# Kernel tuning notes

Measured on AMD Instinct MI355X. Metric: run time of the kernel, lower is better.

The kernel has to match this reference:

```python
import jax, jax.numpy as jnp
import numpy as np
from jax import lax

B, CIN, COUT, H, W = 4, 256, 256, 64, 64
K = 3  # kernel size
PAD = 1
STRIDE = 1


def setup_inputs() -> dict:
    key = jax.random.key(0)
    k1, k2, k3, k4 = jax.random.split(key, 4)
    x = jax.random.normal(k1, (B, CIN, H, W), dtype=jnp.float32)
    # small offset weights so learned offsets are modest (original init is zeros)
    offset_w = jax.random.normal(k2, (3 * K * K, CIN, K, K), dtype=jnp.float32) * 0.01
    offset_b = jax.random.normal(k3, (3 * K * K,), dtype=jnp.float32) * 0.01
    dcn_w = jax.random.normal(k4, (COUT, CIN, K, K), dtype=jnp.float32) * (1.0 / np.sqrt(CIN * K * K))
    return {"x": x, "offset_w": offset_w, "offset_b": offset_b, "dcn_w": dcn_w}


def _dcnv2(x, offset_w, offset_b, dcn_w):
    b, c, h, w = x.shape
    kk = K * K
    # offset conv (standard 3x3, stride 1, pad 1)
    o = lax.conv_general_dilated(
        x, offset_w, (STRIDE, STRIDE), ((PAD, PAD), (PAD, PAD)),
        dimension_numbers=("NCHW", "OIHW", "NCHW"))
    o = o + offset_b[None, :, None, None]
    ho, wo = o.shape[2], o.shape[3]
    off = o[:, : 2 * kk].reshape(b, kk, 2, ho, wo)  # pairs are (dy, dx)
    dy, dx = off[:, :, 0], off[:, :, 1]             # [b,kk,ho,wo]
    mask = jax.nn.sigmoid(o[:, 2 * kk:])            # [b,kk,ho,wo]

    ki, kj = jnp.meshgrid(jnp.arange(K), jnp.arange(K), indexing="ij")
    ki = ki.reshape(kk).astype(jnp.float32)
    kj = kj.reshape(kk).astype(jnp.float32)
    base_y = (jnp.arange(ho, dtype=jnp.float32) * STRIDE - PAD)[None, None, :, None] + ki[None, :, None, None]
    base_x = (jnp.arange(wo, dtype=jnp.float32) * STRIDE - PAD)[None, None, None, :] + kj[None, :, None, None]
    py = base_y + dy  # [b,kk,ho,wo] sampling y
    px = base_x + dx  # sampling x

    y0 = jnp.floor(py)
    x0 = jnp.floor(px)
    wy = py - y0  # bilinear fractional weights
    wx = px - x0
    y0i = y0.astype(jnp.int32)
    x0i = x0.astype(jnp.int32)

    xT = x.transpose(0, 2, 3, 1)  # [b,h,w,c] for channel-last gathers
    bidx = jnp.arange(b)[:, None, None, None]

    def gather(yi, xi):
        # zero padding outside the image
        valid = (yi >= 0) & (yi < h) & (xi >= 0) & (xi < w)
        yc = jnp.clip(yi, 0, h - 1)
        xc = jnp.clip(xi, 0, w - 1)
        v = xT[bidx, yc, xc]  # [b,kk,ho,wo,c]
        return v * valid[..., None].astype(x.dtype)

    g00 = gather(y0i, x0i)
    g01 = gather(y0i, x0i + 1)
    g10 = gather(y0i + 1, x0i)
    g11 = gather(y0i + 1, x0i + 1)

    wy_ = wy[..., None]
    wx_ = wx[..., None]
    sampled = (g00 * (1 - wy_) * (1 - wx_) + g01 * (1 - wy_) * wx_
               + g10 * wy_ * (1 - wx_) + g11 * wy_ * wx_)
    sampled = sampled * mask[..., None]  # modulation

    wk = dcn_w.reshape(dcn_w.shape[0], c, kk)  # [o,c,kk]
    return jnp.einsum("bkhwc,ock->bohw", sampled, wk)


def reference(x, offset_w, offset_b, dcn_w):
    return _dcnv2(x, offset_w, offset_b, dcn_w)
```

## Files before the change

kernel.cpp:

```cpp
#include <hip/hip_runtime.h>
#include <hip/hip_bf16.h>
#include <stdint.h>
#include <math.h>

#define KDIM 2304

typedef __attribute__((ext_vector_type(8))) short bf16x8;
typedef __attribute__((ext_vector_type(4))) float f32x4;

__device__ inline unsigned short f2bf(float f) {
  union { float f; unsigned int u; } v; v.f = f;
  unsigned int u = v.u;
  unsigned int r = (u + 0x7FFFu + ((u >> 16) & 1u)) >> 16;
  return (unsigned short)r;
}
__device__ inline float bf2f(unsigned short h) {
  union { unsigned int u; float f; } v; v.u = ((unsigned int)h) << 16;
  return v.f;
}

__device__ inline void gl2lds16(const void* g, void* l) {
  __builtin_amdgcn_global_load_lds((const __attribute__((address_space(1))) void*)g,
                                   (__attribute__((address_space(3))) void*)l,
                                   16, 0, 0);
}

#define GLOAD16(dst, ptr) \
  asm volatile("global_load_dwordx4 %0, %1, off" : "=v"(dst) : "v"(ptr))

__global__ __launch_bounds__(256) void k_prep(const float* __restrict__ x,
                                              unsigned short* __restrict__ xTb,
                                              const float* __restrict__ dcn_w,
                                              const float* __restrict__ offset_w,
                                              unsigned short* __restrict__ Wpk,
                                              unsigned short* __restrict__ Wob,
                                              unsigned short* __restrict__ zp) {
  __shared__ float tile[32][65];
  int bx = (int)blockIdx.x;
  int t = threadIdx.x;
  if (bx < 2048) {
    int pt = bx & 127, ct = (bx >> 7) & 3, b = bx >> 9;
    int p0 = pt * 32, c0 = ct * 64;
    const float* xb = x + ((size_t)b << 20);
#pragma unroll
    for (int i = 0; i < 2; ++i) {
      int idx = t + i * 256;
      int c = idx >> 3, pq = idx & 7;
      float4 v = *(const float4*)(xb + ((size_t)(c0 + c) << 12) + p0 + pq * 4);
      tile[pq * 4 + 0][c] = v.x;
      tile[pq * 4 + 1][c] = v.y;
      tile[pq * 4 + 2][c] = v.z;
      tile[pq * 4 + 3][c] = v.w;
    }
    __syncthreads();
    unsigned short* ob = xTb + ((size_t)b << 20);
#pragma unroll
    for (int i = 0; i < 2; ++i) {
      int idx = t + i * 256;
      int p = idx >> 4, cg = idx & 15;
      ushort4 o;
      o.x = f2bf(tile[p][cg * 4 + 0]);
      o.y = f2bf(tile[p][cg * 4 + 1]);
      o.z = f2bf(tile[p][cg * 4 + 2]);
      o.w = f2bf(tile[p][cg * 4 + 3]);
      *(ushort4*)(ob + (((size_t)(p0 + p)) << 8) + c0 + cg * 4) = o;
    }
  } else {
    int gid = (bx - 2048) * 256 + t;
    const int N1 = 72 * 8192;
    const int N2 = 32 * KDIM;
    if (gid < N1) {
      int j = gid & 7;
      int lane = (gid >> 3) & 63;
      int mb = (gid >> 9) & 15;
      int kc = gid >> 13;
      int row = mb * 16 + (lane & 15);
      int gk = kc * 32 + ((lane >> 4) << 3) + j;
      int c = gk & 255, kidx = gk >> 8;
      Wpk[gid] = f2bf(dcn_w[((size_t)(row * 256 + c)) * 9 + kidx]);
    } else if (gid < N1 + N2) {
      int g = gid - N1;
      int ch = g / KDIM, k = g % KDIM;
      int kidx = k >> 8, c = k & 255;
      Wob[g] = (ch < 27) ? f2bf(offset_w[((size_t)(ch * 256 + c)) * 9 + kidx])
                         : (unsigned short)0;
    } else if (gid < N1 + N2 + 128) {
      zp[gid - N1 - N2] = 0;
    }
  }
}

__global__ __launch_bounds__(256) void k_offs(const unsigned short* __restrict__ xTb,
                                              const unsigned short* __restrict__ Wob,
                                              const unsigned short* __restrict__ zp,
                                              const float* __restrict__ offb,
                                              float* __restrict__ SW) {
  __shared__ unsigned short As[4][32 * 32];
  __shared__ unsigned short Bs[4][32 * 32];
  __shared__ float Os[32][33];
  int t = threadIdx.x;
  int wv = t >> 6, lane = t & 63;
  int bid = (int)blockIdx.x;
  int swz = (bid & 7) * 64 + (bid >> 3);
  int n0 = swz * 32;

  int r0 = (t >> 2) & 31, coff = (t & 3) * 8;
  int rowA = n0 + r0;
  int b_ = rowA >> 12, hw = rowA & 4095, h = hw >> 6, w = hw & 63;
  int rB = ((t - 128) >> 2) & 31;

  f32x4 acc = {};

  auto stage = [&](int kt) {
    int buf = kt & 3;
    int k0 = kt * 32;
    int kidx = k0 >> 8, c0 = k0 & 255;
    if (t < 128) {
      int di = kidx / 3 - 1, dj = kidx % 3 - 1;
      int y = h + di, xx = w + dj;
      const unsigned short* g = (y >= 0 && y < 64 && xx >= 0 && xx < 64)
          ? xTb + (((((size_t)b_) << 12) + (y << 6) + xx) << 8) + c0 + coff
          : zp;
      gl2lds16(g, (char*)As[buf] + wv * 1024);
    } else {
      const unsigned short* gB = Wob + (size_t)rB * KDIM + k0 + coff;
      gl2lds16(gB, (char*)Bs[buf] + (wv - 2) * 1024);
    }
  };

  stage(0); stage(1); stage(2);

  int mf = wv & 1, nf = wv >> 1;
  for (int kt = 0; kt < 72; ++kt) {
    if (kt <= 69)      asm volatile("s_waitcnt vmcnt(2)" ::: "memory");
    else if (kt == 70) asm volatile("s_waitcnt vmcnt(1)" ::: "memory");
    else               asm volatile("s_waitcnt vmcnt(0)" ::: "memory");
    asm volatile("s_barrier" ::: "memory");
    if (kt + 3 < 72) stage(kt + 3);
    int buf = kt & 3;
    bf16x8 aF = *(const bf16x8*)(As[buf] + (mf * 16 + (lane & 15)) * 32 + (lane >> 4) * 8);
    bf16x8 bF = *(const bf16x8*)(Bs[buf] + (nf * 16 + (lane & 15)) * 32 + (lane >> 4) * 8);
    acc = __builtin_amdgcn_mfma_f32_16x16x32_bf16(aF, bF, acc, 0, 0, 0);
  }

  int quad = lane >> 4, cl = lane & 15;
#pragma unroll
  for (int r = 0; r < 4; ++r)
    Os[mf * 16 + quad * 4 + r][nf * 16 + cl] = acc[r];
  __syncthreads();

  for (int item = t; item < 288; item += 256) {
    int bl = item & 31, k = item >> 5;
    int bhw = n0 + bl;
    int h_ = (bhw >> 6) & 63, w_ = bhw & 63;
    float dy = Os[bl][2 * k]     + offb[2 * k];
    float dx = Os[bl][2 * k + 1] + offb[2 * k + 1];
    float mv = Os[bl][18 + k]    + offb[18 + k];
    float mask = 1.0f / (1.0f + expf(-mv));

    float py = (float)(h_ - 1 + k / 3) + dy;
    float px = (float)(w_ - 1 + k % 3) + dx;
    float y0f = floorf(py), x0f = floorf(px);
    float wy = py - y0f, wx = px - x0f;
    int y0 = (int)y0f, x0 = (int)x0f;
    int y1 = y0 + 1, x1 = x0 + 1;

    float vy0 = (y0 >= 0 && y0 < 64) ? 1.f : 0.f;
    float vy1 = (y1 >= 0 && y1 < 64) ? 1.f : 0.f;
    float vx0 = (x0 >= 0 && x0 < 64) ? 1.f : 0.f;
    float vx1 = (x1 >= 0 && x1 < 64) ? 1.f : 0.f;
    int y0c = min(max(y0, 0), 63), y1c = min(max(y1, 0), 63);
    int x0c = min(max(x0, 0), 63), x1c = min(max(x1, 0), 63);

    float4 wv4;
    wv4.x = (1.f - wy) * (1.f - wx) * vy0 * vx0 * mask;
    wv4.y = (1.f - wy) * wx * vy0 * vx1 * mask;
    wv4.z = wy * (1.f - wx) * vy1 * vx0 * mask;
    wv4.w = wy * wx * vy1 * vx1 * mask;
    uint4 ov;
    ov.x = (unsigned)(((y0c << 6) + x0c) << 8);
    ov.y = (unsigned)(((y0c << 6) + x1c) << 8);
    ov.z = (unsigned)(((y1c << 6) + x0c) << 8);
    ov.w = (unsigned)(((y1c << 6) + x1c) << 8);

    float* p = SW + (size_t)(k * 16384 + bhw) * 8;
    *(float4*)p = wv4;
    *(uint4*)(p + 4) = ov;
  }
}

#define PHASE(PH, Q, AF, BUF, WB, WM)                                          \
  do {                                                                         \
    if (((PH) & 3) == 0) {                                                     \
      int g_ = (PH) >> 2;                                                      \
      wv4 = *(const float4*)(SWL + (size_t)(g_ * 128 + r * 2) * 4);            \
      ov  = *(const uint4*)(SWL + (size_t)(g_ * 128 + r * 2 + 1) * 4);         \
    } else if (((PH) & 3) == 2 && (PH) < 32) {                                 \
      ov  = *(const uint4*)(SWL + (size_t)((((PH) >> 2) + 1) * 128 + r * 2 + 1) * 4); \
    }                                                                          \
    asm volatile("s_waitcnt vmcnt(" #WB ")" ::: "memory");                     \
    __builtin_amdgcn_sched_barrier(0);                                         \
    float s_[8];                                                               \
    _Pragma("unroll")                                                          \
    for (int j_ = 0; j_ < 8; ++j_)                                             \
      s_[j_] = wv4.x * bf2f((unsigned short)Q[0][j_]) +                        \
               wv4.y * bf2f((unsigned short)Q[1][j_]) +                        \
               wv4.z * bf2f((unsigned short)Q[2][j_]) +                        \
               wv4.w * bf2f((unsigned short)Q[3][j_]);                         \
    union { __hip_bfloat162 h2[4]; bf16x8 v; } pk_;                            \
    pk_.h2[0] = __float22bfloat162_rn(make_float2(s_[0], s_[1]));              \
    pk_.h2[1] = __float22bfloat162_rn(make_float2(s_[2], s_[3]));              \
    pk_.h2[2] = __float22bfloat162_rn(make_float2(s_[4], s_[5]));              \
    pk_.h2[3] = __float22bfloat162_rn(make_float2(s_[6], s_[7]));              \
    *(bf16x8*)(&Bs[BUF][s_th][bsw]) = pk_.v;                                   \
    if ((PH) < 34) {                                                           \
      int kn0_ = 2 * (PH) + 4;                                                 \
      unsigned c_ = (unsigned)((((kn0_ & 7) + s_th) << 5) + gg * 8);           \
      GLOAD16(Q[0], xb + ov.x + c_);                                           \
      GLOAD16(Q[1], xb + ov.y + c_);                                           \
      GLOAD16(Q[2], xb + ov.z + c_);                                           \
      GLOAD16(Q[3], xb + ov.w + c_);                                           \
    }                                                                          \
    asm volatile("s_waitcnt vmcnt(" #WM ") lgkmcnt(0)\n\ts_barrier" ::: "memory"); \
    __builtin_amdgcn_sched_barrier(0);                                         \
    _Pragma("unroll")                                                          \
    for (int s2_ = 0; s2_ < 2; ++s2_) {                                        \
      bf16x8 bF0_ = *(const bf16x8*)(                                          \
          &Bs[BUF][s2_][(wn * 32 + (lane & 15)) * 56 + (lane >> 4) * 8]);      \
      bf16x8 bF1_ = *(const bf16x8*)(                                          \
          &Bs[BUF][s2_][(wn * 32 + 16 + (lane & 15)) * 56 + (lane >> 4) * 8]); \
      _Pragma("unroll")                                                        \
      for (int i_ = 0; i_ < 4; ++i_) {                                         \
        acc[i_][0] = __builtin_amdgcn_mfma_f32_16x16x32_bf16(                  \
            AF[s2_ * 4 + i_], bF0_, acc[i_][0], 0, 0, 0);                      \
        acc[i_][1] = __builtin_amdgcn_mfma_f32_16x16x32_bf16(                  \
            AF[s2_ * 4 + i_], bF1_, acc[i_][1], 0, 0, 0);                      \
      }                                                                        \
    }                                                                          \
    if ((PH) < 34) {                                                           \
      _Pragma("unroll")                                                        \
      for (int i_ = 0; i_ < 8; ++i_) {                                         \
        const unsigned short* ap_ =                                            \
            wpBase + ((size_t)((2 * (PH) + 4 + (i_ >> 2)) * 16 + (i_ & 3))) * 512; \
        GLOAD16(AF[i_], ap_);                                                  \
      }                                                                        \
    }                                                                          \
  } while (0)

__global__ __launch_bounds__(512, 2) void k_fused(const unsigned short* __restrict__ Wpk,
                                                  const unsigned short* __restrict__ xTb,
                                                  const float* __restrict__ SW,
                                                  float* __restrict__ out) {
  __shared__ __align__(16) unsigned short Bs[2][2][64 * 56];
  __shared__ __align__(16) float SWL[1152 * 4];
  int t = threadIdx.x;
  int wv = t >> 6, lane = t & 63;
  int wm = wv & 3, wn = wv >> 2;
  int bid = (int)blockIdx.x;
  int swz = (bid & 7) * 32 + (bid >> 3);
  int n0 = swz * 64;
  int b  = n0 >> 12;
  const unsigned short* xb = xTb + ((size_t)b << 20);

  int r = t >> 3;
  int u = t & 7;
  int s_th = u & 1, gg = u >> 1;
  int bsw = r * 56 + gg * 8;

  const unsigned short* wpBase = Wpk + ((size_t)(wm * 4 * 64 + lane)) * 8;

  f32x4 acc[4][2] = {};

  {
#pragma unroll
    for (int i = 0; i < 3; ++i) {
      int hs = t + i * 512;
      if (hs < 1152) {
        int grp = hs >> 7, row = (hs >> 1) & 63, hh = hs & 1;
        const float* src = SW + ((size_t)(grp * 16384 + n0 + row)) * 8 + hh * 4;
        char* dstbase = (char*)SWL + ((size_t)((t & ~63) + i * 512)) * 16;
        gl2lds16(src, dstbase);
      }
    }
  }
  asm volatile("s_waitcnt vmcnt(0)" ::: "memory");
  __builtin_amdgcn_s_barrier();

  float4 wv4; uint4 ov;
  wv4 = *(const float4*)(SWL + (size_t)(r * 2) * 4);
  ov  = *(const uint4*)(SWL + (size_t)(r * 2 + 1) * 4);

  bf16x8 qA[4], qB[4];
  bf16x8 aFA[8], aFB[8];

  {
    unsigned cA = (unsigned)((s_th << 5) + gg * 8);
    GLOAD16(qA[0], xb + ov.x + cA);
    GLOAD16(qA[1], xb + ov.y + cA);
    GLOAD16(qA[2], xb + ov.z + cA);
    GLOAD16(qA[3], xb + ov.w + cA);
#pragma unroll
    for (int i = 0; i < 8; ++i) {
      const unsigned short* ap = wpBase + ((size_t)(((i >> 2)) * 16 + (i & 3))) * 512;
      GLOAD16(aFA[i], ap);
    }
    unsigned cB = (unsigned)(((2 + s_th) << 5) + gg * 8);
    GLOAD16(qB[0], xb + ov.x + cB);
    GLOAD16(qB[1], xb + ov.y + cB);
    GLOAD16(qB[2], xb + ov.z + cB);
    GLOAD16(qB[3], xb + ov.w + cB);
#pragma unroll
    for (int i = 0; i < 8; ++i) {
      const unsigned short* ap = wpBase + ((size_t)((2 + (i >> 2)) * 16 + (i & 3))) * 512;
      GLOAD16(aFB[i], ap);
    }
  }

  for (int ph = 0; ph < 34; ph += 2) {
    PHASE(ph,     qA, aFA, 0, 20, 16);
    PHASE(ph + 1, qB, aFB, 1, 20, 16);
  }
  PHASE(34, qA, aFA, 0, 20, 12);
  PHASE(35, qB, aFB, 1, 8, 0);

  int quad = lane >> 4, cl = lane & 15;
  float* ob = out + (((size_t)b) << 20);
#pragma unroll
  for (int i = 0; i < 4; ++i) {
    int mbase = wm * 64 + i * 16 + quad * 4;
#pragma unroll
    for (int j = 0; j < 2; ++j) {
      int hw = (n0 & 4095) + wn * 32 + j * 16 + cl;
      float* op = ob + hw;
#pragma unroll
      for (int rr = 0; rr < 4; ++rr)
        op[((size_t)(mbase + rr)) << 12] = acc[i][j][rr];
    }
  }
}

extern "C" void kernel_launch(void* const* d_in, const int* in_sizes, int n_in,
                              void* d_out, int out_size, void* d_ws, size_t ws_size,
                              hipStream_t stream) {
  const float* x        = (const float*)d_in[0];
  const float* offset_w = (const float*)d_in[1];
  const float* offset_b = (const float*)d_in[2];
  const float* dcn_w    = (const float*)d_in[3];
  float* out = (float*)d_out;

  char* ws = (char*)d_ws;
  size_t off = 0;
  auto carve = [&](size_t bytes) -> void* {
    void* p = ws + off;
    off += (bytes + 255) & ~(size_t)255;
    return p;
  };
  unsigned short* xTb = (unsigned short*)carve(4ull * 64 * 64 * 256 * 2);
  unsigned short* Wpk = (unsigned short*)carve(72ull * 8192 * 2);
  unsigned short* Wob = (unsigned short*)carve(32ull * KDIM * 2);
  unsigned short* zp  = (unsigned short*)carve(256);
  float*          SW  = (float*)carve(9ull * 16384 * 8 * 4);
  (void)ws_size; (void)in_sizes; (void)n_in; (void)out_size;

  const int WPREP_BLOCKS = (72 * 8192 + 32 * KDIM + 128 + 255) / 256;
  k_prep<<<dim3(2048 + WPREP_BLOCKS), 256, 0, stream>>>(
      x, xTb, dcn_w, offset_w, Wpk, Wob, zp);
  k_offs<<<dim3(512), 256, 0, stream>>>(xTb, Wob, zp, offset_b, SW);
  k_fused<<<dim3(256), 512, 0, stream>>>(Wpk, xTb, SW, out);
}
```

Before: 131.6 us.

## Widen K-step to 128 in fused DCN GEMM and double offset-conv tile

The fused deformable-sampling GEMM now processes 128 channels per phase instead of 64, in 18 phases with one barrier each. Each thread samples 16 channels per phase, and weight-fragment loads are interleaved per 32-channel chunk with finer vmcnt waits. The offset-conv kernel moves to 64-row tiles with 512 threads, 64-wide K steps and an XOR-swizzled LDS layout, halving the block count and barrier count. This cuts synchronization overhead and improves reuse, at the cost of more registers (16 weight fragments, 8 gather registers) and larger LDS use, which may reduce occupancy.

```diff
diff --git a/kernel.cpp b/kernel.cpp
--- a/kernel.cpp
+++ b/kernel.cpp
@@ -27,6 +27,12 @@
 
 #define GLOAD16(dst, ptr) \
   asm volatile("global_load_dwordx4 %0, %1, off" : "=v"(dst) : "v"(ptr))
+
+#define WAITV(N)                                              \
+  do {                                                        \
+    asm volatile("s_waitcnt vmcnt(" #N ")" ::: "memory");     \
+    __builtin_amdgcn_sched_barrier(0);                        \
+  } while (0)
 
 __global__ __launch_bounds__(256) void k_prep(const float* __restrict__ x,
                                               unsigned short* __restrict__ xTb,
@@ -90,57 +96,75 @@
   }
 }
 
-__global__ __launch_bounds__(256) void k_offs(const unsigned short* __restrict__ xTb,
+__global__ __launch_bounds__(512) void k_offs(const unsigned short* __restrict__ xTb,
                                               const unsigned short* __restrict__ Wob,
                                               const unsigned short* __restrict__ zp,
                                               const float* __restrict__ offb,
                                               float* __restrict__ SW) {
-  __shared__ unsigned short As[4][32 * 32];
-  __shared__ unsigned short Bs[4][32 * 32];
-  __shared__ float Os[32][33];
+  __shared__ unsigned short As[4][64 * 64];
+  __shared__ unsigned short Bsf[4][32 * 64];
+  __shared__ float Os[64][33];
   int t = threadIdx.x;
   int wv = t >> 6, lane = t & 63;
   int bid = (int)blockIdx.x;
-  int swz = (bid & 7) * 64 + (bid >> 3);
-  int n0 = swz * 32;
-
-  int r0 = (t >> 2) & 31, coff = (t & 3) * 8;
-  int rowA = n0 + r0;
+  int swz = (bid & 7) * 32 + (bid >> 3);
+  int n0 = swz * 64;
+
+  int ra = t >> 3, ua = t & 7;
+  int kpA = ((ua ^ (ra & 7)) << 3);
+  int rowA = n0 + ra;
   int b_ = rowA >> 12, hw = rowA & 4095, h = hw >> 6, w = hw & 63;
-  int rB = ((t - 128) >> 2) & 31;
+  int rb = (t >> 3) & 31;
+  int kpB = (((t & 7) ^ (rb & 7)) << 3);
 
   f32x4 acc = {};
 
   auto stage = [&](int kt) {
     int buf = kt & 3;
-    int k0 = kt * 32;
+    int k0 = kt * 64;
     int kidx = k0 >> 8, c0 = k0 & 255;
-    if (t < 128) {
+    {
       int di = kidx / 3 - 1, dj = kidx % 3 - 1;
       int y = h + di, xx = w + dj;
       const unsigned short* g = (y >= 0 && y < 64 && xx >= 0 && xx < 64)
-          ? xTb + (((((size_t)b_) << 12) + (y << 6) + xx) << 8) + c0 + coff
+          ? xTb + (((((size_t)b_) << 12) + (y << 6) + xx) << 8) + c0 + kpA
           : zp;
       gl2lds16(g, (char*)As[buf] + wv * 1024);
+    }
+    if (t < 256) {
+      const unsigned short* gB = Wob + (size_t)rb * KDIM + k0 + kpB;
+      gl2lds16(gB, (char*)Bsf[buf] + wv * 1024);
+    }
+  };
+
+  stage(0); stage(1); stage(2);
+
+  int mf = wv & 3, nf = wv >> 2;
+  int arow = mf * 16 + (lane & 15);
+  int brow = nf * 16 + (lane & 15);
+  int q4 = lane >> 4;
+  for (int kt = 0; kt < 36; ++kt) {
+    if (kt <= 33) {
+      if (wv < 4) asm volatile("s_waitcnt vmcnt(4)" ::: "memory");
+      else        asm volatile("s_waitcnt vmcnt(2)" ::: "memory");
+    } else if (kt == 34) {
+      if (wv < 4) asm volatile("s_waitcnt vmcnt(2)" ::: "memory");
+      else        asm volatile("s_waitcnt vmcnt(1)" ::: "memory");
     } else {
-      const unsigned short* gB = Wob + (size_t)rB * KDIM + k0 + coff;
-      gl2lds16(gB, (char*)Bs[buf] + (wv - 2) * 1024);
-    }
-  };
-
-  stage(0); stage(1); stage(2);
-
-  int mf = wv & 1, nf = wv >> 1;
-  for (int kt = 0; kt < 72; ++kt) {
-    if (kt <= 69)      asm volatile("s_waitcnt vmcnt(2)" ::: "memory");
-    else if (kt == 70) asm volatile("s_waitcnt vmcnt(1)" ::: "memory");
-    else               asm volatile("s_waitcnt vmcnt(0)" ::: "memory");
+      asm volatile("s_waitcnt vmcnt(0)" ::: "memory");
+    }
     asm volatile("s_barrier" ::: "memory");
-    if (kt + 3 < 72) stage(kt + 3);
+    if (kt + 3 < 36) stage(kt + 3);
     int buf = kt & 3;
-    bf16x8 aF = *(const bf16x8*)(As[buf] + (mf * 16 + (lane & 15)) * 32 + (lane >> 4) * 8);
-    bf16x8 bF = *(const bf16x8*)(Bs[buf] + (nf * 16 + (lane & 15)) * 32 + (lane >> 4) * 8);
-    acc = __builtin_amdgcn_mfma_f32_16x16x32_bf16(aF, bF, acc, 0, 0, 0);
+#pragma unroll
+    for (int cc = 0; cc < 2; ++cc) {
+      int kq = (cc << 2) + q4;
+      bf16x8 aF = *(const bf16x8*)((const char*)As[buf] +
+                                   arow * 128 + (((kq ^ (arow & 7))) << 4));
+      bf16x8 bF = *(const bf16x8*)((const char*)Bsf[buf] +
+                                   brow * 128 + (((kq ^ (brow & 7))) << 4));
+      acc = __builtin_amdgcn_mfma_f32_16x16x32_bf16(aF, bF, acc, 0, 0, 0);
+    }
   }
 
   int quad = lane >> 4, cl = lane & 15;
@@ -149,8 +173,8 @@
     Os[mf * 16 + quad * 4 + r][nf * 16 + cl] = acc[r];
   __syncthreads();
 
-  for (int item = t; item < 288; item += 256) {
-    int bl = item & 31, k = item >> 5;
+  for (int item = t; item < 576; item += 512) {
+    int bl = item & 63, k = item >> 6;
     int bhw = n0 + bl;
     int h_ = (bhw >> 6) & 63, w_ = bhw & 63;
     float dy = Os[bl][2 * k]     + offb[2 * k];
@@ -189,69 +213,85 @@
   }
 }
 
-#define PHASE(PH, Q, AF, BUF, WB, WM)                                          \
+#define FCHUNK(P, CC, BUF, ISSUE, W)                                           \
   do {                                                                         \
-    if (((PH) & 3) == 0) {                                                     \
-      int g_ = (PH) >> 2;                                                      \
-      wv4 = *(const float4*)(SWL + (size_t)(g_ * 128 + r * 2) * 4);            \
-      ov  = *(const uint4*)(SWL + (size_t)(g_ * 128 + r * 2 + 1) * 4);         \
-    } else if (((PH) & 3) == 2 && (PH) < 32) {                                 \
-      ov  = *(const uint4*)(SWL + (size_t)((((PH) >> 2) + 1) * 128 + r * 2 + 1) * 4); \
+    WAITV(W);                                                                  \
+    bf16x8 bF0_ = *(const bf16x8*)(                                            \
+        &Bs[BUF][(wn * 32 + (lane & 15)) * 136 + (CC) * 32 + (lane >> 4) * 8]);\
+    bf16x8 bF1_ = *(const bf16x8*)(                                            \
+        &Bs[BUF][(wn * 32 + 16 + (lane & 15)) * 136 + (CC) * 32 +              \
+                 (lane >> 4) * 8]);                                            \
+    _Pragma("unroll")                                                          \
+    for (int i_ = 0; i_ < 4; ++i_) {                                           \
+      acc[i_][0] = __builtin_amdgcn_mfma_f32_16x16x32_bf16(                    \
+          aF[(CC) * 4 + i_], bF0_, acc[i_][0], 0, 0, 0);                       \
+      acc[i_][1] = __builtin_amdgcn_mfma_f32_16x16x32_bf16(                    \
+          aF[(CC) * 4 + i_], bF1_, acc[i_][1], 0, 0, 0);                       \
     }                                                                          \
-    asm volatile("s_waitcnt vmcnt(" #WB ")" ::: "memory");                     \
+    if (ISSUE) {                                                               \
+      _Pragma("unroll")                                                        \
+      for (int i_ = 0; i_ < 4; ++i_)                                           \
+        GLOAD16(aF[(CC) * 4 + i_],                                             \
+                wpBase + ((size_t)((((P) + 1) * 4 + (CC)) * 16 + i_)) * 512);  \
+    }                                                                          \
+  } while (0)
+
+#define FPHASE(P, BUF, ISSUE, W0, W1, W2, W3)                                  \
+  do {                                                                         \
+    if ((((P) & 1) == 0) && (P) < 16) {                                        \
+      int g_ = ((P) >> 1) + 1;                                                 \
+      wv4n = *(const float4*)(SWL + (size_t)(g_ * 128 + r * 2) * 4);           \
+      ovn  = *(const uint4*)(SWL + (size_t)(g_ * 128 + r * 2 + 1) * 4);        \
+    }                                                                          \
+    WAITV(16);                                                                 \
+    float s_[16];                                                              \
+    _Pragma("unroll")                                                          \
+    for (int j_ = 0; j_ < 8; ++j_) {                                           \
+      s_[j_] = wv4.x * bf2f((unsigned short)q[0][j_]) +                        \
+               wv4.y * bf2f((unsigned short)q[1][j_]) +                        \
+               wv4.z * bf2f((unsigned short)q[2][j_]) +                        \
+               wv4.w * bf2f((unsigned short)q[3][j_]);                         \
+      s_[8 + j_] = wv4.x * bf2f((unsigned short)q[4][j_]) +                    \
+                   wv4.y * bf2f((unsigned short)q[5][j_]) +                    \
+                   wv4.z * bf2f((unsigned short)q[6][j_]) +                    \
+                   wv4.w * bf2f((unsigned short)q[7][j_]);                     \
+    }                                                                          \
+    union { __hip_bfloat162 h2[4]; bf16x8 v; } pka_, pkb_;                     \
+    pka_.h2[0] = __float22bfloat162_rn(make_float2(s_[0], s_[1]));             \
+    pka_.h2[1] = __float22bfloat162_rn(make_float2(s_[2], s_[3]));             \
+    pka_.h2[2] = __float22bfloat162_rn(make_float2(s_[4], s_[5]));             \
+    pka_.h2[3] = __float22bfloat162_rn(make_float2(s_[6], s_[7]));             \
+    pkb_.h2[0] = __float22bfloat162_rn(make_float2(s_[8], s_[9]));             \
+    pkb_.h2[1] = __float22bfloat162_rn(make_float2(s_[10], s_[11]));           \
+    pkb_.h2[2] = __float22bfloat162_rn(make_float2(s_[12], s_[13]));           \
+    pkb_.h2[3] = __float22bfloat162_rn(make_float2(s_[14], s_[15]));           \
+    *(bf16x8*)(&Bs[BUF][bsw])     = pka_.v;                                    \
+    *(bf16x8*)(&Bs[BUF][bsw + 8]) = pkb_.v;                                    \
+    if (ISSUE) {                                                               \
+      uint4 o_ = (((P) & 1) ? ovn : ov);                                       \
+      unsigned cb_ = (unsigned)((((((P) + 1)) & 1) << 7) + u * 16);            \
+      GLOAD16(q[0], xb + o_.x + cb_);                                          \
+      GLOAD16(q[1], xb + o_.y + cb_);                                          \
+      GLOAD16(q[2], xb + o_.z + cb_);                                          \
+      GLOAD16(q[3], xb + o_.w + cb_);                                          \
+      GLOAD16(q[4], xb + o_.x + cb_ + 8);                                      \
+      GLOAD16(q[5], xb + o_.y + cb_ + 8);                                      \
+      GLOAD16(q[6], xb + o_.z + cb_ + 8);                                      \
+      GLOAD16(q[7], xb + o_.w + cb_ + 8);                                      \
+    }                                                                          \
+    asm volatile("s_waitcnt lgkmcnt(0)\n\ts_barrier" ::: "memory");            \
     __builtin_amdgcn_sched_barrier(0);                                         \
-    float s_[8];                                                               \
-    _Pragma("unroll")                                                          \
-    for (int j_ = 0; j_ < 8; ++j_)                                             \
-      s_[j_] = wv4.x * bf2f((unsigned short)Q[0][j_]) +                        \
-               wv4.y * bf2f((unsigned short)Q[1][j_]) +                        \
-               wv4.z * bf2f((unsigned short)Q[2][j_]) +                        \
-               wv4.w * bf2f((unsigned short)Q[3][j_]);                         \
-    union { __hip_bfloat162 h2[4]; bf16x8 v; } pk_;                            \
-    pk_.h2[0] = __float22bfloat162_rn(make_float2(s_[0], s_[1]));              \
-    pk_.h2[1] = __float22bfloat162_rn(make_float2(s_[2], s_[3]));              \
-    pk_.h2[2] = __float22bfloat162_rn(make_float2(s_[4], s_[5]));              \
-    pk_.h2[3] = __float22bfloat162_rn(make_float2(s_[6], s_[7]));              \
-    *(bf16x8*)(&Bs[BUF][s_th][bsw]) = pk_.v;                                   \
-    if ((PH) < 34) {                                                           \
-      int kn0_ = 2 * (PH) + 4;                                                 \
-      unsigned c_ = (unsigned)((((kn0_ & 7) + s_th) << 5) + gg * 8);           \
-      GLOAD16(Q[0], xb + ov.x + c_);                                           \
-      GLOAD16(Q[1], xb + ov.y + c_);                                           \
-      GLOAD16(Q[2], xb + ov.z + c_);                                           \
-      GLOAD16(Q[3], xb + ov.w + c_);                                           \
-    }                                                                          \
-    asm volatile("s_waitcnt vmcnt(" #WM ") lgkmcnt(0)\n\ts_barrier" ::: "memory"); \
-    __builtin_amdgcn_sched_barrier(0);                                         \
-    _Pragma("unroll")                                                          \
-    for (int s2_ = 0; s2_ < 2; ++s2_) {                                        \
-      bf16x8 bF0_ = *(const bf16x8*)(                                          \
-          &Bs[BUF][s2_][(wn * 32 + (lane & 15)) * 56 + (lane >> 4) * 8]);      \
-      bf16x8 bF1_ = *(const bf16x8*)(                                          \
-          &Bs[BUF][s2_][(wn * 32 + 16 + (lane & 15)) * 56 + (lane >> 4) * 8]); \
-      _Pragma("unroll")                                                        \
-      for (int i_ = 0; i_ < 4; ++i_) {                                         \
-        acc[i_][0] = __builtin_amdgcn_mfma_f32_16x16x32_bf16(                  \
-            AF[s2_ * 4 + i_], bF0_, acc[i_][0], 0, 0, 0);                      \
-        acc[i_][1] = __builtin_amdgcn_mfma_f32_16x16x32_bf16(                  \
-            AF[s2_ * 4 + i_], bF1_, acc[i_][1], 0, 0, 0);                      \
-      }                                                                        \
-    }                                                                          \
-    if ((PH) < 34) {                                                           \
-      _Pragma("unroll")                                                        \
-      for (int i_ = 0; i_ < 8; ++i_) {                                         \
-        const unsigned short* ap_ =                                            \
-            wpBase + ((size_t)((2 * (PH) + 4 + (i_ >> 2)) * 16 + (i_ & 3))) * 512; \
-        GLOAD16(AF[i_], ap_);                                                  \
-      }                                                                        \
-    }                                                                          \
+    FCHUNK(P, 0, BUF, ISSUE, W0);                                              \
+    FCHUNK(P, 1, BUF, ISSUE, W1);                                              \
+    FCHUNK(P, 2, BUF, ISSUE, W2);                                              \
+    FCHUNK(P, 3, BUF, ISSUE, W3);                                              \
   } while (0)
 
 __global__ __launch_bounds__(512, 2) void k_fused(const unsigned short* __restrict__ Wpk,
                                                   const unsigned short* __restrict__ xTb,
                                                   const float* __restrict__ SW,
                                                   float* __restrict__ out) {
-  __shared__ __align__(16) unsigned short Bs[2][2][64 * 56];
+  __shared__ __align__(16) unsigned short Bs[2][64 * 136];
   __shared__ __align__(16) float SWL[1152 * 4];
   int t = threadIdx.x;
   int wv = t >> 6, lane = t & 63;
@@ -264,8 +304,7 @@
 
   int r = t >> 3;
   int u = t & 7;
-  int s_th = u & 1, gg = u >> 1;
-  int bsw = r * 56 + gg * 8;
+  int bsw = r * 136 + u * 16;
 
   const unsigned short* wpBase = Wpk + ((size_t)(wm * 4 * 64 + lane)) * 8;
 
@@ -286,42 +325,38 @@
   asm volatile("s_waitcnt vmcnt(0)" ::: "memory");
   __builtin_amdgcn_s_barrier();
 
-  float4 wv4; uint4 ov;
+  float4 wv4, wv4n; uint4 ov, ovn;
   wv4 = *(const float4*)(SWL + (size_t)(r * 2) * 4);
   ov  = *(const uint4*)(SWL + (size_t)(r * 2 + 1) * 4);
-
-  bf16x8 qA[4], qB[4];
-  bf16x8 aFA[8], aFB[8];
+  wv4n = wv4; ovn = ov;
+
+  bf16x8 q[8];
+  bf16x8 aF[16];
 
   {
-    unsigned cA = (unsigned)((s_th << 5) + gg * 8);
-    GLOAD16(qA[0], xb + ov.x + cA);
-    GLOAD16(qA[1], xb + ov.y + cA);
-    GLOAD16(qA[2], xb + ov.z + cA);
-    GLOAD16(qA[3], xb + ov.w + cA);
-#pragma unroll
-    for (int i = 0; i < 8; ++i) {
-      const unsigned short* ap = wpBase + ((size_t)(((i >> 2)) * 16 + (i & 3))) * 512;
-      GLOAD16(aFA[i], ap);
-    }
-    unsigned cB = (unsigned)(((2 + s_th) << 5) + gg * 8);
-    GLOAD16(qB[0], xb + ov.x + cB);
-    GLOAD16(qB[1], xb + ov.y + cB);
-    GLOAD16(qB[2], xb + ov.z + cB);
-    GLOAD16(qB[3], xb + ov.w + cB);
-#pragma unroll
-    for (int i = 0; i < 8; ++i) {
-      const unsigned short* ap = wpBase + ((size_t)((2 + (i >> 2)) * 16 + (i & 3))) * 512;
-      GLOAD16(aFB[i], ap);
-    }
-  }
-
-  for (int ph = 0; ph < 34; ph += 2) {
-    PHASE(ph,     qA, aFA, 0, 20, 16);
-    PHASE(ph + 1, qB, aFB, 1, 20, 16);
-  }
-  PHASE(34, qA, aFA, 0, 20, 12);
-  PHASE(35, qB, aFB, 1, 8, 0);
+    unsigned cb = (unsigned)(u * 16);
+    GLOAD16(q[0], xb + ov.x + cb);
+    GLOAD16(q[1], xb + ov.y + cb);
+    GLOAD16(q[2], xb + ov.z + cb);
+    GLOAD16(q[3], xb + ov.w + cb);
+    GLOAD16(q[4], xb + ov.x + cb + 8);
+    GLOAD16(q[5], xb + ov.y + cb + 8);
+    GLOAD16(q[6], xb + ov.z + cb + 8);
+    GLOAD16(q[7], xb + ov.w + cb + 8);
+#pragma unroll
+    for (int cc = 0; cc < 4; ++cc)
+#pragma unroll
+      for (int i = 0; i < 4; ++i)
+        GLOAD16(aF[cc * 4 + i], wpBase + ((size_t)(cc * 16 + i)) * 512);
+  }
+
+  for (int p = 0; p < 16; p += 2) {
+    FPHASE(p,     0, 1, 20, 20, 20, 20);
+    FPHASE(p + 1, 1, 1, 20, 20, 20, 20);
+    wv4 = wv4n; ov = ovn;
+  }
+  FPHASE(16, 0, 1, 20, 20, 20, 20);
+  FPHASE(17, 1, 0, 12, 8, 4, 0);
 
   int quad = lane >> 4, cl = lane & 15;
   float* ob = out + (((size_t)b) << 20);
@@ -365,6 +400,6 @@
   const int WPREP_BLOCKS = (72 * 8192 + 32 * KDIM + 128 + 255) / 256;
   k_prep<<<dim3(2048 + WPREP_BLOCKS), 256, 0, stream>>>(
       x, xTb, dcn_w, offset_w, Wpk, Wob, zp);
-  k_offs<<<dim3(512), 256, 0, stream>>>(xTb, Wob, zp, offset_b, SW);
+  k_offs<<<dim3(256), 512, 0, stream>>>(xTb, Wob, zp, offset_b, SW);
   k_fused<<<dim3(256), 512, 0, stream>>>(Wpk, xTb, SW, out);
 }
```

Result: slower. 136.2 us (+3.5%).

## Stage packed weights through triple-buffered LDS instead of per-wave register loads

Applied to the files above, without the earlier changes.

The fused DCN GEMM kernel no longer loads weight fragments from global memory into registers for each wave. It now copies each phase's 32KB weight slab into a triple-buffered LDS area with global_load_lds and reads MFMA A-fragments from LDS, with the vmcnt wait counts retuned to match. This is meant to cut redundant global weight traffic across waves and free registers. In exchange it adds 96KB of LDS per block, which can lower occupancy below the two-blocks-per-CU launch bound, plus LDS read traffic. An extra barrier is also added to the offset-conv loop, and a shared array is renamed.

```diff
diff --git a/kernel.cpp b/kernel.cpp
--- a/kernel.cpp
+++ b/kernel.cpp
@@ -96,7 +96,7 @@
                                               const float* __restrict__ offb,
                                               float* __restrict__ SW) {
   __shared__ unsigned short As[4][32 * 32];
-  __shared__ unsigned short Bs[4][32 * 32];
+  __shared__ unsigned short Bsf[4][32 * 32];
   __shared__ float Os[32][33];
   int t = threadIdx.x;
   int wv = t >> 6, lane = t & 63;
@@ -124,7 +124,7 @@
       gl2lds16(g, (char*)As[buf] + wv * 1024);
     } else {
       const unsigned short* gB = Wob + (size_t)rB * KDIM + k0 + coff;
-      gl2lds16(gB, (char*)Bs[buf] + (wv - 2) * 1024);
+      gl2lds16(gB, (char*)Bsf[buf] + (wv - 2) * 1024);
     }
   };
 
@@ -139,14 +139,16 @@
     if (kt + 3 < 72) stage(kt + 3);
     int buf = kt & 3;
     bf16x8 aF = *(const bf16x8*)(As[buf] + (mf * 16 + (lane & 15)) * 32 + (lane >> 4) * 8);
-    bf16x8 bF = *(const bf16x8*)(Bs[buf] + (nf * 16 + (lane & 15)) * 32 + (lane >> 4) * 8);
+    bf16x8 bF = *(const bf16x8*)(Bsf[buf] + (nf * 16 + (lane & 15)) * 32 + (lane >> 4) * 8);
     acc = __builtin_amdgcn_mfma_f32_16x16x32_bf16(aF, bF, acc, 0, 0, 0);
+
+    asm volatile("s_barrier" ::: "memory");
   }
 
   int quad = lane >> 4, cl = lane & 15;
 #pragma unroll
-  for (int r = 0; r < 4; ++r)
-    Os[mf * 16 + quad * 4 + r][nf * 16 + cl] = acc[r];
+  for (int rr = 0; rr < 4; ++rr)
+    Os[mf * 16 + quad * 4 + rr][nf * 16 + cl] = acc[rr];
   __syncthreads();
 
   for (int item = t; item < 288; item += 256) {
@@ -189,7 +191,7 @@
   }
 }
 
-#define PHASE(PH, Q, AF, BUF, WB, WM)                                          \
+#define PHASE(PH, Q, BUF, WB, WM)                                              \
   do {                                                                         \
     if (((PH) & 3) == 0) {                                                     \
       int g_ = (PH) >> 2;                                                      \
@@ -221,28 +223,38 @@
       GLOAD16(Q[2], xb + ov.z + c_);                                           \
       GLOAD16(Q[3], xb + ov.w + c_);                                           \
     }                                                                          \
+    __builtin_amdgcn_sched_barrier(0);                                         \
+    if ((PH) < 35) {                                                           \
+      const unsigned short* ws_ = Wpk + (size_t)((PH) + 1) * 16384 +           \
+                                  wv * 512 + lane * 8;                         \
+      char* wd_ = (char*)WpkL[((PH) + 1) % 3] + wv * 1024;                     \
+      gl2lds16(ws_,         wd_);                                              \
+      gl2lds16(ws_ + 4096,  wd_ + 8192);                                       \
+      gl2lds16(ws_ + 8192,  wd_ + 16384);                                      \
+      gl2lds16(ws_ + 12288, wd_ + 24576);                                      \
+    }                                                                          \
     asm volatile("s_waitcnt vmcnt(" #WM ") lgkmcnt(0)\n\ts_barrier" ::: "memory"); \
     __builtin_amdgcn_sched_barrier(0);                                         \
-    _Pragma("unroll")                                                          \
-    for (int s2_ = 0; s2_ < 2; ++s2_) {                                        \
-      bf16x8 bF0_ = *(const bf16x8*)(                                          \
-          &Bs[BUF][s2_][(wn * 32 + (lane & 15)) * 56 + (lane >> 4) * 8]);      \
-      bf16x8 bF1_ = *(const bf16x8*)(                                          \
-          &Bs[BUF][s2_][(wn * 32 + 16 + (lane & 15)) * 56 + (lane >> 4) * 8]); \
+    {                                                                          \
+      const unsigned short* wlp_ =                                             \
+          WpkL[(PH) % 3] + ((wm * 4) << 9) + (lane << 3);                      \
       _Pragma("unroll")                                                        \
-      for (int i_ = 0; i_ < 4; ++i_) {                                         \
-        acc[i_][0] = __builtin_amdgcn_mfma_f32_16x16x32_bf16(                  \
-            AF[s2_ * 4 + i_], bF0_, acc[i_][0], 0, 0, 0);                      \
-        acc[i_][1] = __builtin_amdgcn_mfma_f32_16x16x32_bf16(                  \
-            AF[s2_ * 4 + i_], bF1_, acc[i_][1], 0, 0, 0);                      \
-      }                                                                        \
-    }                                                                          \
-    if ((PH) < 34) {                                                           \
-      _Pragma("unroll")                                                        \
-      for (int i_ = 0; i_ < 8; ++i_) {                                         \
-        const unsigned short* ap_ =                                            \
-            wpBase + ((size_t)((2 * (PH) + 4 + (i_ >> 2)) * 16 + (i_ & 3))) * 512; \
-        GLOAD16(AF[i_], ap_);                                                  \
+      for (int s2_ = 0; s2_ < 2; ++s2_) {                                      \
+        bf16x8 aFs_[4];                                                        \
+        _Pragma("unroll")                                                      \
+        for (int i_ = 0; i_ < 4; ++i_)                                         \
+          aFs_[i_] = *(const bf16x8*)(wlp_ + (s2_ * 16 + i_) * 512);           \
+        bf16x8 bF0_ = *(const bf16x8*)(                                        \
+            &Bs[BUF][s2_][(wn * 32 + (lane & 15)) * 56 + (lane >> 4) * 8]);    \
+        bf16x8 bF1_ = *(const bf16x8*)(                                        \
+            &Bs[BUF][s2_][(wn * 32 + 16 + (lane & 15)) * 56 + (lane >> 4) * 8]); \
+        _Pragma("unroll")                                                      \
+        for (int i_ = 0; i_ < 4; ++i_) {                                       \
+          acc[i_][0] = __builtin_amdgcn_mfma_f32_16x16x32_bf16(                \
+              aFs_[i_], bF0_, acc[i_][0], 0, 0, 0);                            \
+          acc[i_][1] = __builtin_amdgcn_mfma_f32_16x16x32_bf16(                \
+              aFs_[i_], bF1_, acc[i_][1], 0, 0, 0);                            \
+        }                                                                      \
       }                                                                        \
     }                                                                          \
   } while (0)
@@ -253,6 +265,7 @@
                                                   float* __restrict__ out) {
   __shared__ __align__(16) unsigned short Bs[2][2][64 * 56];
   __shared__ __align__(16) float SWL[1152 * 4];
+  __shared__ __align__(16) unsigned short WpkL[3][16384];
   int t = threadIdx.x;
   int wv = t >> 6, lane = t & 63;
   int wm = wv & 3, wn = wv >> 2;
@@ -267,8 +280,6 @@
   int s_th = u & 1, gg = u >> 1;
   int bsw = r * 56 + gg * 8;
 
-  const unsigned short* wpBase = Wpk + ((size_t)(wm * 4 * 64 + lane)) * 8;
-
   f32x4 acc[4][2] = {};
 
   {
@@ -291,7 +302,6 @@
   ov  = *(const uint4*)(SWL + (size_t)(r * 2 + 1) * 4);
 
   bf16x8 qA[4], qB[4];
-  bf16x8 aFA[8], aFB[8];
 
   {
     unsigned cA = (unsigned)((s_th << 5) + gg * 8);
@@ -299,29 +309,29 @@
     GLOAD16(qA[1], xb + ov.y + cA);
     GLOAD16(qA[2], xb + ov.z + cA);
     GLOAD16(qA[3], xb + ov.w + cA);
-#pragma unroll
-    for (int i = 0; i < 8; ++i) {
-      const unsigned short* ap = wpBase + ((size_t)(((i >> 2)) * 16 + (i & 3))) * 512;
-      GLOAD16(aFA[i], ap);
-    }
     unsigned cB = (unsigned)(((2 + s_th) << 5) + gg * 8);
     GLOAD16(qB[0], xb + ov.x + cB);
     GLOAD16(qB[1], xb + ov.y + cB);
     GLOAD16(qB[2], xb + ov.z + cB);
     GLOAD16(qB[3], xb + ov.w + cB);
-#pragma unroll
-    for (int i = 0; i < 8; ++i) {
-      const unsigned short* ap = wpBase + ((size_t)((2 + (i >> 2)) * 16 + (i & 3))) * 512;
-      GLOAD16(aFB[i], ap);
-    }
-  }
-
-  for (int ph = 0; ph < 34; ph += 2) {
-    PHASE(ph,     qA, aFA, 0, 20, 16);
-    PHASE(ph + 1, qB, aFB, 1, 20, 16);
-  }
-  PHASE(34, qA, aFA, 0, 20, 12);
-  PHASE(35, qB, aFB, 1, 8, 0);
+    __builtin_amdgcn_sched_barrier(0);
+    const unsigned short* ws = Wpk + wv * 512 + lane * 8;
+    char* wd = (char*)WpkL[0] + wv * 1024;
+    gl2lds16(ws,         wd);
+    gl2lds16(ws + 4096,  wd + 8192);
+    gl2lds16(ws + 8192,  wd + 16384);
+    gl2lds16(ws + 12288, wd + 24576);
+    __builtin_amdgcn_sched_barrier(0);
+  }
+
+  PHASE(0, qA, 0, 8, 8);
+  PHASE(1, qB, 1, 12, 8);
+  for (int ph = 2; ph < 34; ph += 2) {
+    PHASE(ph,     qA, 0, 12, 8);
+    PHASE(ph + 1, qB, 1, 12, 8);
+  }
+  PHASE(34, qA, 0, 12, 4);
+  PHASE(35, qB, 1, 8, 0);
 
   int quad = lane >> 4, cl = lane & 15;
   float* ob = out + (((size_t)b) << 20);
```

New measurement: 132.8 us. Within noise of the previous version (+0.9%).

## Split offset-conv K dimension across waves with per-wave pipelines and LDS reduction

Applied to the files above, without the earlier changes.

The offset convolution GEMM kernel now gives each of the four waves its own 18-step slice of the K dimension. Each wave computes the full 32x32 output tile with four MFMAs per step, using a private triple-buffered LDS pipeline, so the per-iteration block barrier is gone. The partial accumulators are then summed through LDS in the epilogue. This removes 72 block-wide barriers and raises MFMA work per load. In exchange it uses more LDS, adds a cross-wave reduction, and each wave issues four global-to-LDS loads per stage.

```diff
diff --git a/kernel.cpp b/kernel.cpp
--- a/kernel.cpp
+++ b/kernel.cpp
@@ -95,67 +95,84 @@
                                               const unsigned short* __restrict__ zp,
                                               const float* __restrict__ offb,
                                               float* __restrict__ SW) {
-  __shared__ unsigned short As[4][32 * 32];
-  __shared__ unsigned short Bs[4][32 * 32];
-  __shared__ float Os[32][33];
+  __shared__ __align__(16) unsigned short Ab[4][3][1024];
+  __shared__ __align__(16) unsigned short Bb[4][3][1024];
   int t = threadIdx.x;
   int wv = t >> 6, lane = t & 63;
   int bid = (int)blockIdx.x;
   int swz = (bid & 7) * 64 + (bid >> 3);
   int n0 = swz * 32;
 
-  int r0 = (t >> 2) & 31, coff = (t & 3) * 8;
-  int rowA = n0 + r0;
+  int srow = lane & 31;
+  int schunk = lane >> 5;
+  int rowA = n0 + srow;
   int b_ = rowA >> 12, hw = rowA & 4095, h = hw >> 6, w = hw & 63;
-  int rB = ((t - 128) >> 2) & 31;
-
-  f32x4 acc = {};
+
+  int kbase = wv * 18;
 
   auto stage = [&](int kt) {
-    int buf = kt & 3;
-    int k0 = kt * 32;
+    int k0 = (kbase + kt) * 32;
     int kidx = k0 >> 8, c0 = k0 & 255;
-    if (t < 128) {
-      int di = kidx / 3 - 1, dj = kidx % 3 - 1;
-      int y = h + di, xx = w + dj;
-      const unsigned short* g = (y >= 0 && y < 64 && xx >= 0 && xx < 64)
-          ? xTb + (((((size_t)b_) << 12) + (y << 6) + xx) << 8) + c0 + coff
-          : zp;
-      gl2lds16(g, (char*)As[buf] + wv * 1024);
-    } else {
-      const unsigned short* gB = Wob + (size_t)rB * KDIM + k0 + coff;
-      gl2lds16(gB, (char*)Bs[buf] + (wv - 2) * 1024);
-    }
+    int di = kidx / 3 - 1, dj = kidx % 3 - 1;
+    int y = h + di, xx = w + dj;
+    const unsigned short* ga = (y >= 0 && y < 64 && xx >= 0 && xx < 64)
+        ? xTb + (((((size_t)b_) << 12) + (y << 6) + xx) << 8) + c0
+        : zp;
+    char* ad = (char*)Ab[wv][kt % 3];
+    gl2lds16(ga + schunk * 8,        ad);
+    gl2lds16(ga + (2 + schunk) * 8,  ad + 1024);
+    const unsigned short* gb = Wob + (size_t)srow * KDIM + k0;
+    char* bd = (char*)Bb[wv][kt % 3];
+    gl2lds16(gb + schunk * 8,        bd);
+    gl2lds16(gb + (2 + schunk) * 8,  bd + 1024);
   };
 
+  f32x4 a00 = {}, a01 = {}, a10 = {}, a11 = {};
+
   stage(0); stage(1); stage(2);
 
-  int mf = wv & 1, nf = wv >> 1;
-  for (int kt = 0; kt < 72; ++kt) {
-    if (kt <= 69)      asm volatile("s_waitcnt vmcnt(2)" ::: "memory");
-    else if (kt == 70) asm volatile("s_waitcnt vmcnt(1)" ::: "memory");
+  int fo = (lane >> 4) * 256 + (lane & 15) * 8;
+  for (int kt = 0; kt < 18; ++kt) {
+    if (kt <= 15)      asm volatile("s_waitcnt vmcnt(8)" ::: "memory");
+    else if (kt == 16) asm volatile("s_waitcnt vmcnt(4)" ::: "memory");
     else               asm volatile("s_waitcnt vmcnt(0)" ::: "memory");
-    asm volatile("s_barrier" ::: "memory");
-    if (kt + 3 < 72) stage(kt + 3);
-    int buf = kt & 3;
-    bf16x8 aF = *(const bf16x8*)(As[buf] + (mf * 16 + (lane & 15)) * 32 + (lane >> 4) * 8);
-    bf16x8 bF = *(const bf16x8*)(Bs[buf] + (nf * 16 + (lane & 15)) * 32 + (lane >> 4) * 8);
-    acc = __builtin_amdgcn_mfma_f32_16x16x32_bf16(aF, bF, acc, 0, 0, 0);
-  }
-
+    __builtin_amdgcn_sched_barrier(0);
+    const unsigned short* As_ = Ab[wv][kt % 3];
+    const unsigned short* Bs_ = Bb[wv][kt % 3];
+    bf16x8 a0 = *(const bf16x8*)(As_ + fo);
+    bf16x8 a1 = *(const bf16x8*)(As_ + fo + 128);
+    bf16x8 b0 = *(const bf16x8*)(Bs_ + fo);
+    bf16x8 b1 = *(const bf16x8*)(Bs_ + fo + 128);
+    a00 = __builtin_amdgcn_mfma_f32_16x16x32_bf16(a0, b0, a00, 0, 0, 0);
+    a01 = __builtin_amdgcn_mfma_f32_16x16x32_bf16(a0, b1, a01, 0, 0, 0);
+    a10 = __builtin_amdgcn_mfma_f32_16x16x32_bf16(a1, b0, a10, 0, 0, 0);
+    a11 = __builtin_amdgcn_mfma_f32_16x16x32_bf16(a1, b1, a11, 0, 0, 0);
+    __builtin_amdgcn_sched_barrier(0);
+    if (kt + 3 < 18) stage(kt + 3);
+  }
+
+  __syncthreads();
+  float (*Osp)[32][33] = (float(*)[32][33])Ab;
   int quad = lane >> 4, cl = lane & 15;
 #pragma unroll
-  for (int r = 0; r < 4; ++r)
-    Os[mf * 16 + quad * 4 + r][nf * 16 + cl] = acc[r];
+  for (int rr = 0; rr < 4; ++rr) {
+    Osp[wv][quad * 4 + rr][cl]           = a00[rr];
+    Osp[wv][quad * 4 + rr][16 + cl]      = a01[rr];
+    Osp[wv][16 + quad * 4 + rr][cl]      = a10[rr];
+    Osp[wv][16 + quad * 4 + rr][16 + cl] = a11[rr];
+  }
   __syncthreads();
 
   for (int item = t; item < 288; item += 256) {
     int bl = item & 31, k = item >> 5;
     int bhw = n0 + bl;
     int h_ = (bhw >> 6) & 63, w_ = bhw & 63;
-    float dy = Os[bl][2 * k]     + offb[2 * k];
-    float dx = Os[bl][2 * k + 1] + offb[2 * k + 1];
-    float mv = Os[bl][18 + k]    + offb[18 + k];
+    float dy = Osp[0][bl][2 * k] + Osp[1][bl][2 * k] +
+               Osp[2][bl][2 * k] + Osp[3][bl][2 * k] + offb[2 * k];
+    float dx = Osp[0][bl][2 * k + 1] + Osp[1][bl][2 * k + 1] +
+               Osp[2][bl][2 * k + 1] + Osp[3][bl][2 * k + 1] + offb[2 * k + 1];
+    float mv = Osp[0][bl][18 + k] + Osp[1][bl][18 + k] +
+               Osp[2][bl][18 + k] + Osp[3][bl][18 + k] + offb[18 + k];
     float mask = 1.0f / (1.0f + expf(-mv));
 
     float py = (float)(h_ - 1 + k / 3) + dy;
```

Measured after the change: 133.5 us. About the same (+1.4%).
